# Optimization experiments

Hardware: AMD Instinct MI355X
Metric: run time of the kernel (lower is better)

The kernel has to match this reference:

```python
import jax, jax.numpy as jnp
import numpy as np

EMBED, HEADS, LEVELS, POINTS = 256, 8, 1, 4


def setup_inputs():
    key = jax.random.key(0)
    ks = jax.random.split(key, 8)
    B, NQ = 8, 8192
    Hh, Ww = 128, 128
    E, Hn, L, P = EMBED, HEADS, LEVELS, POINTS
    s = 1.0 / np.sqrt(E)
    return dict(
        query=jax.random.normal(ks[0], (B, NQ, E), jnp.float32),
        value=jax.random.normal(ks[1], (B, Hh * Ww, E), jnp.float32),
        ref_2d=jax.random.uniform(ks[2], (B, NQ, L, 2), dtype=jnp.float32),
        spatial_shapes=jnp.array([[Hh, Ww]], dtype=jnp.int32),
        W_off=jax.random.normal(ks[3], (E, Hn * L * P * 2), jnp.float32) * 0.01,
        b_off=jax.random.normal(ks[4], (Hn * L * P * 2,), jnp.float32) * 0.5,
        W_attn=jax.random.normal(ks[5], (E, Hn * L * P), jnp.float32) * s,
        b_attn=jnp.zeros((Hn * L * P,), jnp.float32),
        W_val=jax.random.normal(ks[6], (E, E), jnp.float32) * s,
        b_val=jnp.zeros((E,), jnp.float32),
        W_out=jax.random.normal(ks[7], (E, E), jnp.float32) * s,
        b_out=jnp.zeros((E,), jnp.float32),
    )


def _bilinear_sample(v, loc, Hl, Wl):
    # v: (B, Hn, Hl*Wl, dh); loc: (B, Hn, NQ, P, 2) normalized [0,1] (x, y)
    B, Hn, NQ, P, _ = loc.shape
    dh = v.shape[-1]
    # torch grid_sample(align_corners=False) pixel coords: p = loc * size - 0.5
    x = loc[..., 0] * Wl - 0.5
    y = loc[..., 1] * Hl - 0.5
    x0 = jnp.floor(x); y0 = jnp.floor(y)
    x1 = x0 + 1.0; y1 = y0 + 1.0
    wx1 = x - x0; wx0 = 1.0 - wx1
    wy1 = y - y0; wy0 = 1.0 - wy1

    def corner(xc, yc, w):
        valid = (xc >= 0) & (xc < Wl) & (yc >= 0) & (yc < Hl)  # zeros padding
        xi = jnp.clip(xc, 0, Wl - 1).astype(jnp.int32)
        yi = jnp.clip(yc, 0, Hl - 1).astype(jnp.int32)
        idx = (yi * Wl + xi).reshape(B, Hn, NQ * P, 1)
        vals = jnp.take_along_axis(v, idx, axis=2).reshape(B, Hn, NQ, P, dh)
        return vals * (w * valid.astype(v.dtype))[..., None]

    return (corner(x0, y0, wx0 * wy0) + corner(x1, y0, wx1 * wy0)
            + corner(x0, y1, wx0 * wy1) + corner(x1, y1, wx1 * wy1))


def _forward(query, value, ref_2d, W_off, b_off, W_attn, b_attn, W_val, b_val, W_out, b_out, shapes):
    B, NQ, E = query.shape
    Hn, L, P = HEADS, LEVELS, POINTS
    dh = E // Hn
    NV = value.shape[1]
    identity = query
    v = (value @ W_val + b_val).reshape(B, NV, Hn, dh)
    off = (query @ W_off + b_off).reshape(B, NQ, Hn, L, P, 2)
    attn = jax.nn.softmax((query @ W_attn + b_attn).reshape(B, NQ, Hn, L * P), axis=-1)
    attn = attn.reshape(B, NQ, Hn, L, P)
    # offset_normalizer = (W, H) per level
    norm = jnp.asarray(shapes[:, ::-1].copy(), dtype=query.dtype)
    loc = ref_2d[:, :, None, :, None, :] + off / norm[None, None, None, :, None, :]
    loc = jnp.transpose(loc, (0, 2, 1, 3, 4, 5))   # (B, Hn, NQ, L, P, 2)
    attn_t = jnp.transpose(attn, (0, 2, 1, 3, 4))  # (B, Hn, NQ, L, P)
    v_t = jnp.transpose(v, (0, 2, 1, 3))           # (B, Hn, NV, dh)
    starts = np.concatenate([[0], np.cumsum(shapes[:, 0] * shapes[:, 1])]).astype(np.int64)
    out = jnp.zeros((B, Hn, NQ, dh), query.dtype)
    for l in range(L):  # static small loop over feature levels
        Hl, Wl = int(shapes[l, 0]), int(shapes[l, 1])
        v_l = v_t[:, :, int(starts[l]):int(starts[l + 1]), :]
        samp = _bilinear_sample(v_l, loc[:, :, :, l], Hl, Wl)  # (B,Hn,NQ,P,dh)
        out = out + jnp.sum(samp * attn_t[:, :, :, l, :, None], axis=3)
    out = jnp.transpose(out, (0, 2, 1, 3)).reshape(B, NQ, E)
    # dropout is identity at eval time
    return out @ W_out + b_out + identity


def reference(query, value, ref_2d, spatial_shapes, W_off, b_off, W_attn, b_attn, W_val, b_val, W_out, b_out):
    shapes = np.asarray(jax.device_get(spatial_shapes))  # static level shapes
    return _forward(query, value, ref_2d, W_off, b_off, W_attn, b_attn, W_val, b_val, W_out, b_out, shapes)
```

## Files before the change

### kernel.cpp

```cpp
#include <hip/hip_runtime.h>

typedef short s16x8 __attribute__((ext_vector_type(8)));
typedef float f32x4 __attribute__((ext_vector_type(4)));

#define HN 8
#define PP 4
#define DH 32
#define NQc 8192
#define NVc 16384
#define EE 256
#define HWc 128

__device__ __forceinline__ unsigned short f2bf(float x) {
  unsigned u = __float_as_uint(x);
  u += 0x7FFF + ((u >> 16) & 1);
  return (unsigned short)(u >> 16);
}

__global__ __launch_bounds__(256) void wprep(
    const float* __restrict__ Wval, const float* __restrict__ Wout,
    const float* __restrict__ Woff, const float* __restrict__ Wattn,
    const float* __restrict__ boff, const float* __restrict__ battn,
    unsigned short* __restrict__ wvt, unsigned short* __restrict__ wot,
    unsigned short* __restrict__ wct, float* __restrict__ bcat) {
  int g = blockIdx.x * 256 + threadIdx.x;
  if (g < 65536) {
    int n = g >> 8, k = g & 255;
    wvt[n * 256 + k] = f2bf(Wval[k * 256 + n]);
  } else if (g < 131072) {
    int g2 = g - 65536;
    int n = g2 >> 8, k = g2 & 255;
    wot[n * 256 + k] = f2bf(Wout[k * 256 + n]);
  } else if (g < 163840) {
    int g2 = g - 131072;
    int n = g2 >> 8, k = g2 & 255;
    float v = 0.f;
    if (n < 64) v = Woff[k * 64 + n];
    else if (n < 96) v = Wattn[k * 32 + (n - 64)];
    wct[n * 256 + k] = f2bf(v);
  } else if (g < 163968) {
    int c = g - 163840;
    bcat[c] = (c < 64) ? boff[c] : ((c < 96) ? battn[c - 64] : 0.f);
  }
}

#define MODE_VAL 0
#define MODE_PLAIN 1
#define MODE_OUT 2

template <int MODE, bool ABF16>
__global__ __launch_bounds__(256) void mfma_gemm(
    const void* __restrict__ Ain, const unsigned short* __restrict__ Wt,
    const float* __restrict__ bias, const float* __restrict__ resid,
    float* __restrict__ out, int ldw) {
  __shared__ unsigned short As[128 * 40];
  __shared__ unsigned short Ws[128 * 40];
  const int t = threadIdx.x;
  const int lane = t & 63, wave = t >> 6;
  const int lane15 = lane & 15, quad = lane >> 4;
  const int wr = wave >> 1, wc = wave & 1;
  const int bm = blockIdx.x * 128, bn = blockIdx.y * 128;

  f32x4 acc[4][4];
#pragma unroll
  for (int i = 0; i < 4; ++i)
#pragma unroll
    for (int j = 0; j < 4; ++j)
#pragma unroll
      for (int r = 0; r < 4; ++r) acc[i][j][r] = 0.f;

  for (int k0 = 0; k0 < 256; k0 += 32) {
    float4 av[4];
    uint4 av2[2];
    uint4 wv[2];
    if (!ABF16) {
      const float* Af = (const float*)Ain;
#pragma unroll
      for (int i = 0; i < 4; ++i) {
        int row = i * 32 + (t >> 3);
        av[i] = *(const float4*)(Af + (size_t)(bm + row) * 256 + k0 + (t & 7) * 4);
      }
    } else {
      const unsigned short* Ab = (const unsigned short*)Ain;
#pragma unroll
      for (int i = 0; i < 2; ++i) {
        int s = i * 256 + t;
        av2[i] = *(const uint4*)(Ab + (size_t)(bm + (s >> 2)) * 256 + k0 + (s & 3) * 8);
      }
    }
#pragma unroll
    for (int i = 0; i < 2; ++i) {
      int s = i * 256 + t;
      wv[i] = *(const uint4*)(Wt + (size_t)(bn + (s >> 2)) * 256 + k0 + (s & 3) * 8);
    }
    __syncthreads();
    if (!ABF16) {
#pragma unroll
      for (int i = 0; i < 4; ++i) {
        int row = i * 32 + (t >> 3);
        ushort4 c;
        c.x = f2bf(av[i].x); c.y = f2bf(av[i].y); c.z = f2bf(av[i].z); c.w = f2bf(av[i].w);
        *(ushort4*)&As[row * 40 + (t & 7) * 4] = c;
      }
    } else {
#pragma unroll
      for (int i = 0; i < 2; ++i) {
        int s = i * 256 + t;
        *(uint4*)&As[(s >> 2) * 40 + (s & 3) * 8] = av2[i];
      }
    }
#pragma unroll
    for (int i = 0; i < 2; ++i) {
      int s = i * 256 + t;
      *(uint4*)&Ws[(s >> 2) * 40 + (s & 3) * 8] = wv[i];
    }
    __syncthreads();
    s16x8 af[4], bfr[4];
#pragma unroll
    for (int tm = 0; tm < 4; ++tm)
      af[tm] = *(const s16x8*)&As[(wr * 64 + tm * 16 + lane15) * 40 + quad * 8];
#pragma unroll
    for (int tn = 0; tn < 4; ++tn)
      bfr[tn] = *(const s16x8*)&Ws[(wc * 64 + tn * 16 + lane15) * 40 + quad * 8];
#pragma unroll
    for (int tm = 0; tm < 4; ++tm)
#pragma unroll
      for (int tn = 0; tn < 4; ++tn)
        acc[tm][tn] = __builtin_amdgcn_mfma_f32_16x16x32_bf16(af[tm], bfr[tn], acc[tm][tn], 0, 0, 0);
  }

#pragma unroll
  for (int tm = 0; tm < 4; ++tm) {
#pragma unroll
    for (int tn = 0; tn < 4; ++tn) {
      const int col = bn + wc * 64 + tn * 16 + lane15;
      const float bcol = bias[col];
#pragma unroll
      for (int r = 0; r < 4; ++r) {
        const int row = bm + wr * 64 + tm * 16 + quad * 4 + r;
        float v = acc[tm][tn][r] + bcol;
        if (MODE == MODE_VAL) {
          const int b = row >> 14, n = row & (NVc - 1);
          const int h = col >> 5, d = col & 31;
          out[(((size_t)(b * HN + h) * NVc + n) * DH) + d] = v;
        } else if (MODE == MODE_PLAIN) {
          out[(size_t)row * ldw + col] = v;
        } else {
          const size_t off = (size_t)row * 256 + col;
          out[off] = v + resid[off];
        }
      }
    }
  }
}

__global__ __launch_bounds__(256) void prep_points(
    const float* __restrict__ oa, const float* __restrict__ ref2d,
    unsigned int* __restrict__ meta) {
  const int g = blockIdx.x * 256 + threadIdx.x;
  const int bq = g >> 3, h = g & 7;
  const float* oarow = oa + (size_t)bq * 128;
  const float rx = ref2d[(size_t)bq * 2 + 0];
  const float ry = ref2d[(size_t)bq * 2 + 1];

  const float l0 = oarow[64 + h * 4 + 0];
  const float l1 = oarow[64 + h * 4 + 1];
  const float l2 = oarow[64 + h * 4 + 2];
  const float l3 = oarow[64 + h * 4 + 3];
  const float mx = fmaxf(fmaxf(l0, l1), fmaxf(l2, l3));
  float ee[4];
  ee[0] = expf(l0 - mx); ee[1] = expf(l1 - mx); ee[2] = expf(l2 - mx); ee[3] = expf(l3 - mx);
  const float inv = 1.0f / (ee[0] + ee[1] + ee[2] + ee[3]);

  unsigned int* m = meta + (size_t)g * 20;
#pragma unroll
  for (int p = 0; p < PP; ++p) {
    const float a = ee[p] * inv;
    const float ox = oarow[h * 8 + p * 2 + 0];
    const float oy = oarow[h * 8 + p * 2 + 1];
    const float x = (rx + ox * (1.0f / HWc)) * (float)HWc - 0.5f;
    const float y = (ry + oy * (1.0f / HWc)) * (float)HWc - 0.5f;
    const float x0f = floorf(x), y0f = floorf(y);
    const int x0 = (int)x0f, y0 = (int)y0f;
    const float wx1 = x - x0f, wx0 = 1.f - wx1;
    const float wy1 = y - y0f, wy0 = 1.f - wy1;
    const bool vx0 = (unsigned)x0 < (unsigned)HWc, vx1 = (unsigned)(x0 + 1) < (unsigned)HWc;
    const bool vy0 = (unsigned)y0 < (unsigned)HWc, vy1 = (unsigned)(y0 + 1) < (unsigned)HWc;
    const int xi0 = min(max(x0, 0), HWc - 1), xi1 = min(max(x0 + 1, 0), HWc - 1);
    const int yi0 = min(max(y0, 0), HWc - 1), yi1 = min(max(y0 + 1, 0), HWc - 1);
    m[p] = (unsigned)xi0 | ((unsigned)yi0 << 8) | ((unsigned)xi1 << 16) | ((unsigned)yi1 << 24);
    float4 w;
    w.x = (vx0 && vy0) ? a * wx0 * wy0 : 0.f;
    w.y = (vx1 && vy0) ? a * wx1 * wy0 : 0.f;
    w.z = (vx0 && vy1) ? a * wx0 * wy1 : 0.f;
    w.w = (vx1 && vy1) ? a * wx1 * wy1 : 0.f;
    *(float4*)&m[4 + p * 4] = w;
  }
}

__global__ __launch_bounds__(256) void sample_kernel(
    const float* __restrict__ vbuf,
    const unsigned int* __restrict__ meta,
    unsigned short* __restrict__ outs) {
  const int t = threadIdx.x;
  const int d = t & 31;
  const int ql = t >> 5;
  const int sl = blockIdx.x >> 10;
  const int qc = blockIdx.x & 1023;
  const int b = sl >> 3;
  const int h = sl & 7;
  const int q = qc * 8 + ql;
  const size_t bq = (size_t)b * NQc + q;
  const unsigned int* m = meta + ((size_t)bq * 8 + h) * 20;
  const uint4 pk = *(const uint4*)m;
  const float* vb = vbuf + (size_t)sl * (NVc * DH) + d;

  float acc = 0.f;
#pragma unroll
  for (int p = 0; p < PP; ++p) {
    const unsigned P = (p == 0) ? pk.x : (p == 1) ? pk.y : (p == 2) ? pk.z : pk.w;
    const float4 w = *(const float4*)(m + 4 + p * 4);
    const int x0 = P & 255, y0 = (P >> 8) & 255, x1 = (P >> 16) & 255, y1 = P >> 24;
    const int r0 = y0 << 12, r1 = y1 << 12;
    acc += w.x * vb[r0 + (x0 << 5)];
    acc += w.y * vb[r0 + (x1 << 5)];
    acc += w.z * vb[r1 + (x0 << 5)];
    acc += w.w * vb[r1 + (x1 << 5)];
  }
  outs[bq * EE + h * DH + d] = f2bf(acc);
}

extern "C" void kernel_launch(void* const* d_in, const int* in_sizes, int n_in,
                              void* d_out, int out_size, void* d_ws, size_t ws_size,
                              hipStream_t stream) {
  const float* query = (const float*)d_in[0];
  const float* value = (const float*)d_in[1];
  const float* ref2d = (const float*)d_in[2];
  const float* Woff  = (const float*)d_in[4];
  const float* boff  = (const float*)d_in[5];
  const float* Wattn = (const float*)d_in[6];
  const float* battn = (const float*)d_in[7];
  const float* Wval  = (const float*)d_in[8];
  const float* bval  = (const float*)d_in[9];
  const float* Wout  = (const float*)d_in[10];
  const float* bout  = (const float*)d_in[11];
  float* out = (float*)d_out;
  float* ws = (float*)d_ws;

  float* vbuf = ws;
  float* oa_s = vbuf + 33554432;
  unsigned int* meta = (unsigned int*)(oa_s + 8388608);
  unsigned short* wvt = (unsigned short*)(meta + 10485760);
  unsigned short* wot = wvt + 65536;
  unsigned short* wct = wot + 65536;
  float* bcat = (float*)(wct + 32768);

  wprep<<<641, 256, 0, stream>>>(Wval, Wout, Woff, Wattn, boff, battn, wvt, wot, wct, bcat);

  mfma_gemm<MODE_VAL, false><<<dim3(1024, 2), 256, 0, stream>>>(
      (const void*)value, wvt, bval, nullptr, vbuf, 256);

  mfma_gemm<MODE_PLAIN, false><<<dim3(512, 1), 256, 0, stream>>>(
      (const void*)query, wct, bcat, nullptr, oa_s, 128);

  prep_points<<<2048, 256, 0, stream>>>(oa_s, ref2d, meta);

  sample_kernel<<<65536, 256, 0, stream>>>(vbuf, meta, (unsigned short*)oa_s);

  mfma_gemm<MODE_OUT, true><<<dim3(512, 2), 256, 0, stream>>>(
      (const void*)oa_s, wot, bout, query, out, 256);
}
```

Before: 508.3 us.

## Store projected values in bf16, fuse point prep into GEMM, stage epilogues via LDS

The value projection now writes bf16 into the per-head layout through an LDS-staged transpose with 16-byte stores, which halves the value buffer traffic seen by the gather-heavy sampler. The offset/attention GEMM computes the softmax and bilinear corner metadata directly in its epilogue, so the separate prep_points kernel and its round trip through global memory go away. The output GEMM stages tiles in LDS so the residual add uses coalesced float4 accesses. The trade-offs are bf16 rounding of the sampled values, larger shared-memory footprints that may reduce occupancy, and a fast __expf in the softmax.

Result: faster. 439.7 us (-13.5%).

```diff
diff --git a/kernel.cpp b/kernel.cpp
--- a/kernel.cpp
+++ b/kernel.cpp
@@ -15,6 +15,9 @@
   unsigned u = __float_as_uint(x);
   u += 0x7FFF + ((u >> 16) & 1);
   return (unsigned short)(u >> 16);
+}
+__device__ __forceinline__ float bf2f(unsigned short h) {
+  return __uint_as_float(((unsigned)h) << 16);
 }
 
 __global__ __launch_bounds__(256) void wprep(
@@ -48,13 +51,20 @@
 #define MODE_PLAIN 1
 #define MODE_OUT 2
 
+template <int MODE>
+struct SmemBytes { static constexpr int v = 36864; };
+template <> struct SmemBytes<MODE_PLAIN> { static constexpr int v = 49664; };
+template <> struct SmemBytes<MODE_OUT>   { static constexpr int v = 33792; };
+
 template <int MODE, bool ABF16>
 __global__ __launch_bounds__(256) void mfma_gemm(
     const void* __restrict__ Ain, const unsigned short* __restrict__ Wt,
     const float* __restrict__ bias, const float* __restrict__ resid,
-    float* __restrict__ out, int ldw) {
-  __shared__ unsigned short As[128 * 40];
-  __shared__ unsigned short Ws[128 * 40];
+    const float* __restrict__ ref2d, unsigned int* __restrict__ meta,
+    void* __restrict__ outp) {
+  __shared__ __align__(16) char smem[SmemBytes<MODE>::v];
+  unsigned short* As = (unsigned short*)smem;
+  unsigned short* Ws = As + 128 * 40;
   const int t = threadIdx.x;
   const int lane = t & 63, wave = t >> 6;
   const int lane15 = lane & 15, quad = lane >> 4;
@@ -69,51 +79,38 @@
 #pragma unroll
       for (int r = 0; r < 4; ++r) acc[i][j][r] = 0.f;
 
+  const int ar = t >> 3, ac = (t & 7) * 4;
+  const int wr2 = t >> 1, wcp = (t & 1) * 2;
+
   for (int k0 = 0; k0 < 256; k0 += 32) {
     float4 av[4];
-    uint4 av2[2];
-    uint4 wv[2];
+    uint4 ab0, ab1;
     if (!ABF16) {
       const float* Af = (const float*)Ain;
 #pragma unroll
-      for (int i = 0; i < 4; ++i) {
-        int row = i * 32 + (t >> 3);
-        av[i] = *(const float4*)(Af + (size_t)(bm + row) * 256 + k0 + (t & 7) * 4);
-      }
+      for (int i = 0; i < 4; ++i)
+        av[i] = *(const float4*)(Af + (size_t)(bm + ar + i * 32) * 256 + k0 + ac);
     } else {
       const unsigned short* Ab = (const unsigned short*)Ain;
-#pragma unroll
-      for (int i = 0; i < 2; ++i) {
-        int s = i * 256 + t;
-        av2[i] = *(const uint4*)(Ab + (size_t)(bm + (s >> 2)) * 256 + k0 + (s & 3) * 8);
-      }
-    }
-#pragma unroll
-    for (int i = 0; i < 2; ++i) {
-      int s = i * 256 + t;
-      wv[i] = *(const uint4*)(Wt + (size_t)(bn + (s >> 2)) * 256 + k0 + (s & 3) * 8);
-    }
+      ab0 = *(const uint4*)(Ab + (size_t)(bm + wr2) * 256 + k0 + wcp * 8);
+      ab1 = *(const uint4*)(Ab + (size_t)(bm + wr2) * 256 + k0 + wcp * 8 + 8);
+    }
+    uint4 wv0 = *(const uint4*)(Wt + (size_t)(bn + wr2) * 256 + k0 + wcp * 8);
+    uint4 wv1 = *(const uint4*)(Wt + (size_t)(bn + wr2) * 256 + k0 + wcp * 8 + 8);
     __syncthreads();
     if (!ABF16) {
 #pragma unroll
       for (int i = 0; i < 4; ++i) {
-        int row = i * 32 + (t >> 3);
         ushort4 c;
         c.x = f2bf(av[i].x); c.y = f2bf(av[i].y); c.z = f2bf(av[i].z); c.w = f2bf(av[i].w);
-        *(ushort4*)&As[row * 40 + (t & 7) * 4] = c;
+        *(ushort4*)&As[(ar + i * 32) * 40 + ac] = c;
       }
     } else {
-#pragma unroll
-      for (int i = 0; i < 2; ++i) {
-        int s = i * 256 + t;
-        *(uint4*)&As[(s >> 2) * 40 + (s & 3) * 8] = av2[i];
-      }
-    }
-#pragma unroll
-    for (int i = 0; i < 2; ++i) {
-      int s = i * 256 + t;
-      *(uint4*)&Ws[(s >> 2) * 40 + (s & 3) * 8] = wv[i];
-    }
+      *(uint4*)&As[wr2 * 40 + wcp * 8] = ab0;
+      *(uint4*)&As[wr2 * 40 + wcp * 8 + 8] = ab1;
+    }
+    *(uint4*)&Ws[wr2 * 40 + wcp * 8] = wv0;
+    *(uint4*)&Ws[wr2 * 40 + wcp * 8 + 8] = wv1;
     __syncthreads();
     s16x8 af[4], bfr[4];
 #pragma unroll
@@ -129,77 +126,131 @@
         acc[tm][tn] = __builtin_amdgcn_mfma_f32_16x16x32_bf16(af[tm], bfr[tn], acc[tm][tn], 0, 0, 0);
   }
 
-#pragma unroll
-  for (int tm = 0; tm < 4; ++tm) {
-#pragma unroll
-    for (int tn = 0; tn < 4; ++tn) {
-      const int col = bn + wc * 64 + tn * 16 + lane15;
-      const float bcol = bias[col];
-#pragma unroll
-      for (int r = 0; r < 4; ++r) {
-        const int row = bm + wr * 64 + tm * 16 + quad * 4 + r;
-        float v = acc[tm][tn][r] + bcol;
-        if (MODE == MODE_VAL) {
-          const int b = row >> 14, n = row & (NVc - 1);
-          const int h = col >> 5, d = col & 31;
-          out[(((size_t)(b * HN + h) * NVc + n) * DH) + d] = v;
-        } else if (MODE == MODE_PLAIN) {
-          out[(size_t)row * ldw + col] = v;
-        } else {
-          const size_t off = (size_t)row * 256 + col;
-          out[off] = v + resid[off];
+  if (MODE == MODE_VAL) {
+    unsigned short* Ct = (unsigned short*)smem;
+    __syncthreads();
+#pragma unroll
+    for (int tm = 0; tm < 4; ++tm)
+#pragma unroll
+      for (int tn = 0; tn < 4; ++tn) {
+        const int coll = wc * 64 + tn * 16 + lane15;
+        const float bcol = bias[bn + coll];
+#pragma unroll
+        for (int r = 0; r < 4; ++r) {
+          const int rowl = wr * 64 + tm * 16 + quad * 4 + r;
+          Ct[rowl * 144 + coll] = f2bf(acc[tm][tn][r] + bcol);
         }
       }
+    __syncthreads();
+    unsigned short* outs = (unsigned short*)outp;
+    const int b = bm >> 14, n0 = bm & (NVc - 1), hbase = bn >> 5;
+#pragma unroll
+    for (int i = 0; i < 8; ++i) {
+      const int id = i * 256 + t;
+      const int h4 = id >> 9, rem = id & 511, n = rem >> 2, c4 = rem & 3;
+      uint4 v = *(const uint4*)&Ct[n * 144 + h4 * 32 + c4 * 8];
+      *(uint4*)(outs + (((size_t)(b * HN + hbase + h4) * NVc + n0 + n) * DH + c4 * 8)) = v;
+    }
+  } else if (MODE == MODE_PLAIN) {
+    float* Cf = (float*)smem;
+    __syncthreads();
+#pragma unroll
+    for (int tm = 0; tm < 4; ++tm)
+#pragma unroll
+      for (int tn = 0; tn < 4; ++tn) {
+        const int coll = wc * 64 + tn * 16 + lane15;
+        if (coll < 96) {
+          const float bcol = bias[coll];
+#pragma unroll
+          for (int r = 0; r < 4; ++r) {
+            const int rowl = wr * 64 + tm * 16 + quad * 4 + r;
+            Cf[rowl * 97 + coll] = acc[tm][tn][r] + bcol;
+          }
+        }
+      }
+    __syncthreads();
+#pragma unroll
+    for (int i = 0; i < 4; ++i) {
+      const int task = i * 256 + t;
+      const int h = task & 7, rowl = task >> 3;
+      const int bq = bm + rowl;
+      const float* row = Cf + rowl * 97;
+      const float rx = ref2d[(size_t)bq * 2 + 0];
+      const float ry = ref2d[(size_t)bq * 2 + 1];
+      const float l0 = row[64 + h * 4 + 0], l1 = row[64 + h * 4 + 1];
+      const float l2 = row[64 + h * 4 + 2], l3 = row[64 + h * 4 + 3];
+      const float mx = fmaxf(fmaxf(l0, l1), fmaxf(l2, l3));
+      float e0 = __expf(l0 - mx), e1 = __expf(l1 - mx), e2 = __expf(l2 - mx), e3 = __expf(l3 - mx);
+      const float inv = 1.0f / (e0 + e1 + e2 + e3);
+      float ee[4] = {e0, e1, e2, e3};
+      unsigned int* m = meta + ((size_t)bq * 8 + h) * 20;
+      uint4 pk;
+      float4 wts[4];
+#pragma unroll
+      for (int p = 0; p < PP; ++p) {
+        const float a = ee[p] * inv;
+        const float ox = row[h * 8 + p * 2 + 0];
+        const float oy = row[h * 8 + p * 2 + 1];
+        const float x = (rx + ox * (1.0f / HWc)) * (float)HWc - 0.5f;
+        const float y = (ry + oy * (1.0f / HWc)) * (float)HWc - 0.5f;
+        const float x0f = floorf(x), y0f = floorf(y);
+        const int x0 = (int)x0f, y0 = (int)y0f;
+        const float wx1 = x - x0f, wx0 = 1.f - wx1;
+        const float wy1 = y - y0f, wy0 = 1.f - wy1;
+        const bool vx0 = (unsigned)x0 < (unsigned)HWc, vx1 = (unsigned)(x0 + 1) < (unsigned)HWc;
+        const bool vy0 = (unsigned)y0 < (unsigned)HWc, vy1 = (unsigned)(y0 + 1) < (unsigned)HWc;
+        const int xi0 = min(max(x0, 0), HWc - 1), xi1 = min(max(x0 + 1, 0), HWc - 1);
+        const int yi0 = min(max(y0, 0), HWc - 1), yi1 = min(max(y0 + 1, 0), HWc - 1);
+        const unsigned pv = (unsigned)xi0 | ((unsigned)yi0 << 8) | ((unsigned)xi1 << 16) | ((unsigned)yi1 << 24);
+        if (p == 0) pk.x = pv; else if (p == 1) pk.y = pv; else if (p == 2) pk.z = pv; else pk.w = pv;
+        float4 w;
+        w.x = (vx0 && vy0) ? a * wx0 * wy0 : 0.f;
+        w.y = (vx1 && vy0) ? a * wx1 * wy0 : 0.f;
+        w.z = (vx0 && vy1) ? a * wx0 * wy1 : 0.f;
+        w.w = (vx1 && vy1) ? a * wx1 * wy1 : 0.f;
+        wts[p] = w;
+      }
+      *(uint4*)m = pk;
+#pragma unroll
+      for (int p = 0; p < PP; ++p) *(float4*)&m[4 + p * 4] = wts[p];
+    }
+  } else {
+    float* Cf = (float*)smem;
+    float* outf = (float*)outp;
+#pragma unroll
+    for (int pass = 0; pass < 2; ++pass) {
+      __syncthreads();
+      if (wr == pass) {
+#pragma unroll
+        for (int tm = 0; tm < 4; ++tm)
+#pragma unroll
+          for (int tn = 0; tn < 4; ++tn) {
+            const int coll = wc * 64 + tn * 16 + lane15;
+            const float bcol = bias[bn + coll];
+#pragma unroll
+            for (int r = 0; r < 4; ++r) {
+              const int rowl = tm * 16 + quad * 4 + r;
+              Cf[rowl * 132 + coll] = acc[tm][tn][r] + bcol;
+            }
+          }
+      }
+      __syncthreads();
+#pragma unroll
+      for (int i = 0; i < 8; ++i) {
+        const int id = i * 256 + t;
+        const int n = id >> 5, c = id & 31;
+        const size_t row = (size_t)bm + pass * 64 + n;
+        float4 v = *(const float4*)&Cf[n * 132 + c * 4];
+        float4 rs = *(const float4*)(resid + row * 256 + bn + c * 4);
+        v.x += rs.x; v.y += rs.y; v.z += rs.z; v.w += rs.w;
+        *(float4*)(outf + row * 256 + bn + c * 4) = v;
+      }
     }
   }
 }
 
-__global__ __launch_bounds__(256) void prep_points(
-    const float* __restrict__ oa, const float* __restrict__ ref2d,
-    unsigned int* __restrict__ meta) {
-  const int g = blockIdx.x * 256 + threadIdx.x;
-  const int bq = g >> 3, h = g & 7;
-  const float* oarow = oa + (size_t)bq * 128;
-  const float rx = ref2d[(size_t)bq * 2 + 0];
-  const float ry = ref2d[(size_t)bq * 2 + 1];
-
-  const float l0 = oarow[64 + h * 4 + 0];
-  const float l1 = oarow[64 + h * 4 + 1];
-  const float l2 = oarow[64 + h * 4 + 2];
-  const float l3 = oarow[64 + h * 4 + 3];
-  const float mx = fmaxf(fmaxf(l0, l1), fmaxf(l2, l3));
-  float ee[4];
-  ee[0] = expf(l0 - mx); ee[1] = expf(l1 - mx); ee[2] = expf(l2 - mx); ee[3] = expf(l3 - mx);
-  const float inv = 1.0f / (ee[0] + ee[1] + ee[2] + ee[3]);
-
-  unsigned int* m = meta + (size_t)g * 20;
-#pragma unroll
-  for (int p = 0; p < PP; ++p) {
-    const float a = ee[p] * inv;
-    const float ox = oarow[h * 8 + p * 2 + 0];
-    const float oy = oarow[h * 8 + p * 2 + 1];
-    const float x = (rx + ox * (1.0f / HWc)) * (float)HWc - 0.5f;
-    const float y = (ry + oy * (1.0f / HWc)) * (float)HWc - 0.5f;
-    const float x0f = floorf(x), y0f = floorf(y);
-    const int x0 = (int)x0f, y0 = (int)y0f;
-    const float wx1 = x - x0f, wx0 = 1.f - wx1;
-    const float wy1 = y - y0f, wy0 = 1.f - wy1;
-    const bool vx0 = (unsigned)x0 < (unsigned)HWc, vx1 = (unsigned)(x0 + 1) < (unsigned)HWc;
-    const bool vy0 = (unsigned)y0 < (unsigned)HWc, vy1 = (unsigned)(y0 + 1) < (unsigned)HWc;
-    const int xi0 = min(max(x0, 0), HWc - 1), xi1 = min(max(x0 + 1, 0), HWc - 1);
-    const int yi0 = min(max(y0, 0), HWc - 1), yi1 = min(max(y0 + 1, 0), HWc - 1);
-    m[p] = (unsigned)xi0 | ((unsigned)yi0 << 8) | ((unsigned)xi1 << 16) | ((unsigned)yi1 << 24);
-    float4 w;
-    w.x = (vx0 && vy0) ? a * wx0 * wy0 : 0.f;
-    w.y = (vx1 && vy0) ? a * wx1 * wy0 : 0.f;
-    w.z = (vx0 && vy1) ? a * wx0 * wy1 : 0.f;
-    w.w = (vx1 && vy1) ? a * wx1 * wy1 : 0.f;
-    *(float4*)&m[4 + p * 4] = w;
-  }
-}
-
 __global__ __launch_bounds__(256) void sample_kernel(
-    const float* __restrict__ vbuf,
+    const unsigned short* __restrict__ vbuf,
     const unsigned int* __restrict__ meta,
     unsigned short* __restrict__ outs) {
   const int t = threadIdx.x;
@@ -213,7 +264,7 @@
   const size_t bq = (size_t)b * NQc + q;
   const unsigned int* m = meta + ((size_t)bq * 8 + h) * 20;
   const uint4 pk = *(const uint4*)m;
-  const float* vb = vbuf + (size_t)sl * (NVc * DH) + d;
+  const unsigned short* vb = vbuf + (size_t)sl * (NVc * DH) + d;
 
   float acc = 0.f;
 #pragma unroll
@@ -222,10 +273,10 @@
     const float4 w = *(const float4*)(m + 4 + p * 4);
     const int x0 = P & 255, y0 = (P >> 8) & 255, x1 = (P >> 16) & 255, y1 = P >> 24;
     const int r0 = y0 << 12, r1 = y1 << 12;
-    acc += w.x * vb[r0 + (x0 << 5)];
-    acc += w.y * vb[r0 + (x1 << 5)];
-    acc += w.z * vb[r1 + (x0 << 5)];
-    acc += w.w * vb[r1 + (x1 << 5)];
+    acc += w.x * bf2f(vb[r0 + (x0 << 5)]);
+    acc += w.y * bf2f(vb[r0 + (x1 << 5)]);
+    acc += w.z * bf2f(vb[r1 + (x0 << 5)]);
+    acc += w.w * bf2f(vb[r1 + (x1 << 5)]);
   }
   outs[bq * EE + h * DH + d] = f2bf(acc);
 }
@@ -245,28 +296,25 @@
   const float* Wout  = (const float*)d_in[10];
   const float* bout  = (const float*)d_in[11];
   float* out = (float*)d_out;
-  float* ws = (float*)d_ws;
-
-  float* vbuf = ws;
-  float* oa_s = vbuf + 33554432;
-  unsigned int* meta = (unsigned int*)(oa_s + 8388608);
-  unsigned short* wvt = (unsigned short*)(meta + 10485760);
-  unsigned short* wot = wvt + 65536;
-  unsigned short* wct = wot + 65536;
-  float* bcat = (float*)(wct + 32768);
+
+  unsigned short* vbuf = (unsigned short*)d_ws;
+  unsigned int* meta   = (unsigned int*)(vbuf + 33554432);
+  unsigned short* sbuf = (unsigned short*)(meta + 10485760);
+  unsigned short* wvt  = sbuf + 16777216;
+  unsigned short* wot  = wvt + 65536;
+  unsigned short* wct  = wot + 65536;
+  float* bcat          = (float*)(wct + 32768);
 
   wprep<<<641, 256, 0, stream>>>(Wval, Wout, Woff, Wattn, boff, battn, wvt, wot, wct, bcat);
 
   mfma_gemm<MODE_VAL, false><<<dim3(1024, 2), 256, 0, stream>>>(
-      (const void*)value, wvt, bval, nullptr, vbuf, 256);
+      (const void*)value, wvt, bval, nullptr, nullptr, nullptr, (void*)vbuf);
 
   mfma_gemm<MODE_PLAIN, false><<<dim3(512, 1), 256, 0, stream>>>(
-      (const void*)query, wct, bcat, nullptr, oa_s, 128);
-
-  prep_points<<<2048, 256, 0, stream>>>(oa_s, ref2d, meta);
-
-  sample_kernel<<<65536, 256, 0, stream>>>(vbuf, meta, (unsigned short*)oa_s);
+      (const void*)query, wct, bcat, nullptr, ref2d, meta, nullptr);
+
+  sample_kernel<<<65536, 256, 0, stream>>>(vbuf, meta, sbuf);
 
   mfma_gemm<MODE_OUT, true><<<dim3(512, 2), 256, 0, stream>>>(
-      (const void*)oa_s, wot, bout, query, out, 256);
-}
+      (const void*)sbuf, wot, bout, query, nullptr, nullptr, (void*)out);
+}
```
